# Optimization experiments

Measured on AMD Instinct MI355X. Metric: run time of the kernel, lower is better.

## Reference

```python
import jax, jax.numpy as jnp
import numpy as np

BN_EPS = 1e-5
W_BITS = 2
A_BITS = 2


def _quantize_k(x, k):
    # uniform quantization of x in [0,1] to k bits, straight-through estimator
    n = float(2 ** k - 1)
    q = jnp.round(x * n) / n
    return x + jax.lax.stop_gradient(q - x)


def _quant_weight(w, k):
    # DoReFa-style weight quantization to [-1, 1]
    t = jnp.tanh(w)
    t = t / (2.0 * jnp.max(jnp.abs(t))) + 0.5
    return 2.0 * _quantize_k(t, k) - 1.0


def _quant_act(x, k):
    # DoReFa-style activation quantization: clamp to [0,1], quantize
    return _quantize_k(jnp.clip(x, 0.0, 1.0), k)


def _conv3x3(x, w, stride=1):
    # x: [N,C,H,W], w: [O,I,3,3], padding=1
    return jax.lax.conv_general_dilated(
        x, w, window_strides=(stride, stride), padding=((1, 1), (1, 1)),
        dimension_numbers=('NCHW', 'OIHW', 'NCHW'))


def _bn(x, gamma, beta, mean, var):
    inv = gamma / jnp.sqrt(var + BN_EPS)           # [C]
    return x * inv[None, :, None, None] + (beta - mean * inv)[None, :, None, None]


def setup_inputs() -> dict:
    key = jax.random.key(0)
    ks = jax.random.split(key, 8)
    N, C, H, W = 64, 256, 28, 28
    x = jax.random.normal(ks[0], (N, C, H, W), dtype=jnp.float32)
    w1 = jax.random.normal(ks[1], (C, C, 3, 3), dtype=jnp.float32) * 0.05
    w2 = jax.random.normal(ks[2], (C, C, 3, 3), dtype=jnp.float32) * 0.05
    g1 = jnp.ones((C,), jnp.float32)
    b1 = jnp.zeros((C,), jnp.float32)
    m1 = jax.random.normal(ks[3], (C,), dtype=jnp.float32) * 0.1
    v1 = jax.random.uniform(ks[4], (C,), dtype=jnp.float32) + 0.5
    g2 = jnp.ones((C,), jnp.float32)
    b2 = jnp.zeros((C,), jnp.float32)
    m2 = jax.random.normal(ks[5], (C,), dtype=jnp.float32) * 0.1
    v2 = jax.random.uniform(ks[6], (C,), dtype=jnp.float32) + 0.5
    return {'x': x, 'w1': w1, 'g1': g1, 'b1': b1, 'm1': m1, 'v1': v1,
            'w2': w2, 'g2': g2, 'b2': b2, 'm2': m2, 'v2': v2}


def reference(x, w1, g1, b1, m1, v1, w2, g2, b2, m2, v2):
    residual = x
    # conv1 (2-bit quantized weights & activations) -> bn1 -> relu
    out = _conv3x3(_quant_act(x, A_BITS), _quant_weight(w1, W_BITS), stride=1)
    out = jax.nn.relu(_bn(out, g1, b1, m1, v1))
    # conv2 (2-bit quantized) -> bn2
    out = _conv3x3(_quant_act(out, A_BITS), _quant_weight(w2, W_BITS), stride=1)
    out = _bn(out, g2, b2, m2, v2)
    # residual add + relu
    return jax.nn.relu(out + residual)
```

## Files before the change

kernel.cpp:

```cpp
#include <hip/hip_runtime.h>


#define ABUF 14745600
using i32x4 = __attribute__((ext_vector_type(4))) int;

__device__ __forceinline__ void gload16(const void* g, void* l) {
  typedef const __attribute__((address_space(1))) unsigned int* gp_t;
  typedef __attribute__((address_space(3))) unsigned int* lp_t;
  __builtin_amdgcn_global_load_lds((gp_t)g, (lp_t)l, 16, 0, 0);
}

__global__ void prep_bn(const float* g1, const float* b1, const float* m1, const float* v1,
                        const float* g2, const float* b2, const float* m2, const float* v2,
                        float* s1, float* t1, float* s2, float* t2) {
  int c = threadIdx.x;
  float i1 = g1[c] / sqrtf(v1[c] + 1e-5f);
  s1[c] = i1 * (1.f / 9.f);
  t1[c] = b1[c] - m1[c] * i1;
  float i2 = g2[c] / sqrtf(v2[c] + 1e-5f);
  s2[c] = i2 * (1.f / 9.f);
  t2[c] = b2[c] - m2[c] * i2;
}

__global__ void maxabs_k(const float* __restrict__ w1, const float* __restrict__ w2,
                         unsigned* mx) {
  const float4* v = (const float4*)(blockIdx.y ? w2 : w1);
  float loc = 0.f;
  for (int i = blockIdx.x * 256 + threadIdx.x; i < 147456; i += 65536) {
    float4 f = v[i];
    loc = fmaxf(loc, fmaxf(fmaxf(fabsf(f.x), fabsf(f.y)), fmaxf(fabsf(f.z), fabsf(f.w))));
  }
  #pragma unroll
  for (int off = 32; off; off >>= 1) loc = fmaxf(loc, __shfl_xor(loc, off));
  __shared__ float red[4];
  if ((threadIdx.x & 63) == 0) red[threadIdx.x >> 6] = loc;
  __syncthreads();
  if (threadIdx.x == 0) {
    loc = fmaxf(fmaxf(red[0], red[1]), fmaxf(red[2], red[3]));
    atomicMax(&mx[blockIdx.y], __float_as_uint(loc));
  }
}

__global__ void wquant_k(const float* __restrict__ w1, const float* __restrict__ w2,
                         const unsigned* __restrict__ mx,
                         signed char* __restrict__ wq1, signed char* __restrict__ wq2) {
  const float* w = blockIdx.y ? w2 : w1;
  signed char* o = blockIdx.y ? wq2 : wq1;
  int idx = blockIdx.x * 256 + threadIdx.x;
  int oo = idx / 2304, rr = idx % 2304, t9 = rr >> 8, ci = rr & 255;
  float mt = tanhf(__uint_as_float(mx[blockIdx.y]));
  float t = tanhf(w[oo * 2304 + ci * 9 + t9]) / (2.f * mt) + 0.5f;
  int q = (int)rintf(t * 3.f);
  o[idx] = (signed char)(2 * q - 3);
}

__global__ void aquant_k(const float* __restrict__ x, unsigned char* __restrict__ a1) {
  int n = blockIdx.x / 28, h = blockIdx.x % 28;
  __shared__ __align__(16) unsigned char l[28 * 256];
  int c = threadIdx.x;
  const float4* src = (const float4*)(x + (size_t)(n * 256 + c) * 784 + h * 28);
  #pragma unroll
  for (int i = 0; i < 7; ++i) {
    float4 f = src[i];
    int p = i * 4;
    l[(p + 0) * 256 + c] = (unsigned char)(int)rintf(3.f * fminf(fmaxf(f.x, 0.f), 1.f));
    l[(p + 1) * 256 + c] = (unsigned char)(int)rintf(3.f * fminf(fmaxf(f.y, 0.f), 1.f));
    l[(p + 2) * 256 + c] = (unsigned char)(int)rintf(3.f * fminf(fmaxf(f.z, 0.f), 1.f));
    l[(p + 3) * 256 + c] = (unsigned char)(int)rintf(3.f * fminf(fmaxf(f.w, 0.f), 1.f));
  }
  __syncthreads();
  if (threadIdx.x < 224) {
    int p = threadIdx.x >> 3, q = threadIdx.x & 7;
    const uint4* s = (const uint4*)&l[p * 256 + q * 32];
    uint4 v0 = s[0], v1 = s[1];
    unsigned char* dst = a1 + ((size_t)((n * 30 + h + 1) * 30) + (p + 1)) * 256 + q * 32;
    ((uint4*)dst)[0] = v0;
    ((uint4*)dst)[1] = v1;
  }
}

template <int MODE>
__global__ __launch_bounds__(256, 2) void conv_gemm(
    const unsigned char* __restrict__ act, const signed char* __restrict__ wq,
    const float* __restrict__ sC, const float* __restrict__ tC,
    const float* __restrict__ xres, unsigned char* __restrict__ actout,
    float* __restrict__ fout) {
  __shared__ __align__(16) unsigned char lds[32768];
  const int tid = threadIdx.x;
  const int wv = tid >> 6, lane = tid & 63;
  const int pixBase = blockIdx.x * 128;
  const int wchBase = blockIdx.y * 128;

  int pA[4];
  const signed char* wp[4];
  #pragma unroll
  for (int c = 0; c < 4; ++c) {
    int row = wv * 32 + c * 8 + (lane >> 3);
    int k16 = ((lane & 7) ^ (row & 7)) << 4;
    int m = pixBase + row;
    int n = m / 784, rem = m % 784;
    int hh = rem / 28, ww = rem % 28;
    pA[c] = (((n * 30 + hh) * 30 + ww) << 8) + k16;
    wp[c] = wq + (wchBase + row) * 2304 + k16;
  }

  i32x4 acc[4][4];
  #pragma unroll
  for (int i = 0; i < 4; ++i)
    #pragma unroll
    for (int j = 0; j < 4; ++j) acc[i][j] = (i32x4){0, 0, 0, 0};

  const int prow_off = (MODE == 0) ? (wv & 1) * 64 : (wv >> 1) * 64;
  const int wrow_off = (MODE == 0) ? (wv >> 1) * 64 : (wv & 1) * 64;

  for (int ks = 0; ks < 18; ++ks) {
    const int tap = ks >> 1;
    const int toff = (((tap / 3) * 30 + (tap % 3)) << 8) + ((ks & 1) << 7);
    #pragma unroll
    for (int c = 0; c < 4; ++c) {
      gload16(act + pA[c] + toff, &lds[wv * 4096 + c * 1024]);
      gload16(wp[c] + ks * 128, &lds[16384 + wv * 4096 + c * 1024]);
    }
    __syncthreads();

    i32x4 pf[4][2], wf[4][2];
    #pragma unroll
    for (int f = 0; f < 4; ++f) {
      #pragma unroll
      for (int kc = 0; kc < 2; ++kc) {
        int sl = kc * 4 + (lane >> 4);
        int rp = prow_off + f * 16 + (lane & 15);
        pf[f][kc] = *(const i32x4*)&lds[rp * 128 + ((sl ^ (rp & 7)) << 4)];
        int rw = wrow_off + f * 16 + (lane & 15);
        wf[f][kc] = *(const i32x4*)&lds[16384 + rw * 128 + ((sl ^ (rw & 7)) << 4)];
      }
    }
    #pragma unroll
    for (int kc = 0; kc < 2; ++kc)
      #pragma unroll
      for (int i = 0; i < 4; ++i)
        #pragma unroll
        for (int j = 0; j < 4; ++j) {
          if (MODE == 0)
            acc[i][j] = __builtin_amdgcn_mfma_i32_16x16x64_i8(pf[i][kc], wf[j][kc], acc[i][j], 0, 0, 0);
          else
            acc[i][j] = __builtin_amdgcn_mfma_i32_16x16x64_i8(wf[i][kc], pf[j][kc], acc[i][j], 0, 0, 0);
        }
    __syncthreads();
  }

  if (MODE == 0) {
    #pragma unroll
    for (int j = 0; j < 4; ++j) {
      int c = wchBase + wrow_off + j * 16 + (lane & 15);
      float s = sC[c], t = tC[c];
      #pragma unroll
      for (int i = 0; i < 4; ++i) {
        #pragma unroll
        for (int r = 0; r < 4; ++r) {
          int m = pixBase + prow_off + i * 16 + ((lane >> 4) << 2) + r;
          int n = m / 784, rem = m % 784, hh = rem / 28, ww = rem % 28;
          float y = (float)acc[i][j][r] * s + t;
          y = fminf(fmaxf(y, 0.f), 1.f);
          actout[((n * 30 + hh + 1) * 30 + (ww + 1)) * 256 + c] =
              (unsigned char)(int)rintf(y * 3.f);
        }
      }
    }
  } else {
    #pragma unroll
    for (int i = 0; i < 4; ++i) {
      #pragma unroll
      for (int r = 0; r < 4; ++r) {
        int c = wchBase + wrow_off + i * 16 + ((lane >> 4) << 2) + r;
        float s = sC[c], t = tC[c];
        #pragma unroll
        for (int j = 0; j < 4; ++j) {
          int m = pixBase + prow_off + j * 16 + (lane & 15);
          int n = m / 784, rem = m % 784;
          int addr = n * 200704 + c * 784 + rem;
          float y = (float)acc[i][j][r] * s + t + xres[addr];
          fout[addr] = fmaxf(y, 0.f);
        }
      }
    }
  }
}

extern "C" void kernel_launch(void* const* d_in, const int* in_sizes, int n_in,
                              void* d_out, int out_size, void* d_ws, size_t ws_size,
                              hipStream_t stream) {
  const float* x  = (const float*)d_in[0];
  const float* w1 = (const float*)d_in[1];
  const float* g1 = (const float*)d_in[2];
  const float* b1 = (const float*)d_in[3];
  const float* m1 = (const float*)d_in[4];
  const float* v1 = (const float*)d_in[5];
  const float* w2 = (const float*)d_in[6];
  const float* g2 = (const float*)d_in[7];
  const float* b2 = (const float*)d_in[8];
  const float* m2 = (const float*)d_in[9];
  const float* v2 = (const float*)d_in[10];

  char* ws = (char*)d_ws;
  unsigned* mx = (unsigned*)ws;
  float* s1 = (float*)(ws + 1024);
  float* t1 = (float*)(ws + 2048);
  float* s2 = (float*)(ws + 3072);
  float* t2 = (float*)(ws + 4096);
  unsigned char* a1 = (unsigned char*)(ws + 8192);
  unsigned char* a2 = a1 + ABUF;
  signed char* wq1 = (signed char*)(a2 + ABUF);
  signed char* wq2 = wq1 + 589824;

  hipMemsetAsync(ws, 0, 8192 + 2 * (size_t)ABUF, stream);
  prep_bn<<<1, 256, 0, stream>>>(g1, b1, m1, v1, g2, b2, m2, v2, s1, t1, s2, t2);
  maxabs_k<<<dim3(256, 2), 256, 0, stream>>>(w1, w2, mx);
  wquant_k<<<dim3(2304, 2), 256, 0, stream>>>(w1, w2, mx, wq1, wq2);
  aquant_k<<<64 * 28, 256, 0, stream>>>(x, a1);
  conv_gemm<0><<<dim3(392, 2), 256, 0, stream>>>(a1, wq1, s1, t1, nullptr, a2, nullptr);
  conv_gemm<1><<<dim3(392, 2), 256, 0, stream>>>(a2, wq2, s2, t2, x, nullptr, (float*)d_out);
}
```

Measured before the change: 219.9 us.

## Rewrite conv GEMM as 256x256 double-buffered tile with priority-scheduled phases

Result: slower. 224.7 us (+2.2%).

```diff
diff --git a/kernel.cpp b/kernel.cpp
--- a/kernel.cpp
+++ b/kernel.cpp
@@ -52,6 +52,24 @@
   float t = tanhf(w[oo * 2304 + ci * 9 + t9]) / (2.f * mt) + 0.5f;
   int q = (int)rintf(t * 3.f);
   o[idx] = (signed char)(2 * q - 3);
+}
+
+__global__ void border_zero(unsigned char* __restrict__ a1, unsigned char* __restrict__ a2) {
+  int b = blockIdx.x;
+  unsigned char* base = (b >= 64 ? a2 : a1) + (size_t)(b & 63) * 230400;
+  int tid = threadIdx.x;
+  #pragma unroll
+  for (int it = 0; it < 8; ++it) {
+    int pi = it * 16 + (tid >> 4);
+    if (pi < 116) {
+      int hh, ww;
+      if (pi < 30)      { hh = 0;       ww = pi; }
+      else if (pi < 60) { hh = 29;      ww = pi - 30; }
+      else if (pi < 88) { hh = pi - 59; ww = 0; }
+      else              { hh = pi - 87; ww = 29; }
+      *(uint4*)(base + (hh * 30 + ww) * 256 + (tid & 15) * 16) = uint4{0, 0, 0, 0};
+    }
+  }
 }
 
 __global__ void aquant_k(const float* __restrict__ x, unsigned char* __restrict__ a1) {
@@ -79,104 +97,180 @@
   }
 }
 
+#define PH_MID() do { __builtin_amdgcn_s_barrier(); \
+  asm volatile("s_waitcnt lgkmcnt(0)" ::: "memory"); \
+  __builtin_amdgcn_sched_barrier(0); \
+  __builtin_amdgcn_s_setprio(1); } while (0)
+#define PH_END() do { __builtin_amdgcn_s_setprio(0); \
+  __builtin_amdgcn_s_barrier(); } while (0)
+#define PH_ENDV(N) do { __builtin_amdgcn_s_setprio(0); \
+  asm volatile("s_waitcnt vmcnt(" #N ")" ::: "memory"); \
+  __builtin_amdgcn_sched_barrier(0); \
+  __builtin_amdgcn_s_barrier(); } while (0)
+
 template <int MODE>
-__global__ __launch_bounds__(256, 2) void conv_gemm(
+__global__ __launch_bounds__(512, 2) void conv_gemm(
     const unsigned char* __restrict__ act, const signed char* __restrict__ wq,
     const float* __restrict__ sC, const float* __restrict__ tC,
     const float* __restrict__ xres, unsigned char* __restrict__ actout,
     float* __restrict__ fout) {
-  __shared__ __align__(16) unsigned char lds[32768];
-  const int tid = threadIdx.x;
-  const int wv = tid >> 6, lane = tid & 63;
-  const int pixBase = blockIdx.x * 128;
-  const int wchBase = blockIdx.y * 128;
-
-  int pA[4];
-  const signed char* wp[4];
+  extern __shared__ __align__(16) char lds[];
+  const int tid = threadIdx.x, wv = tid >> 6, lane = tid & 63;
+  const int pixBase = blockIdx.x * 256;
+  const int wvm = wv >> 2, wvn = wv & 3;
+  constexpr int RAoff = (MODE == 0) ? 0 : 32768;
+  constexpr int RBoff = 32768 - RAoff;
+
+  int pixB[2][2], wB[2][2];
+  {
+    int s = (lane & 7) ^ ((lane >> 3) & 7);
+    #pragma unroll
+    for (int h = 0; h < 2; ++h)
+      #pragma unroll
+      for (int c = 0; c < 2; ++c) {
+        int r = h * 128 + c * 64 + wv * 8 + (lane >> 3);
+        int p = pixBase + r;
+        int n = p / 784, rem = p % 784, hh = rem / 28, ww = rem % 28;
+        pixB[h][c] = (((n * 30 + hh) * 30 + ww) << 8) + (s << 4);
+        wB[h][c] = r * 2304 + (s << 4);
+      }
+  }
+  auto tof = [](int kt) {
+    int tap = kt >> 1;
+    return ((tap / 3) * 30 + (tap % 3)) * 256 + ((kt & 1) << 7);
+  };
+  auto stagePix = [&](int h, int kt) {
+    const int base = (kt & 1) * 65536 + h * 16384 + wv * 1024;
+    const int toff = tof(kt);
+    gload16(act + pixB[h][0] + toff, &lds[base]);
+    gload16(act + pixB[h][1] + toff, &lds[base + 8192]);
+  };
+  auto stageW = [&](int h, int kt) {
+    const int base = (kt & 1) * 65536 + 32768 + h * 16384 + wv * 1024;
+    gload16(wq + wB[h][0] + kt * 128, &lds[base]);
+    gload16(wq + wB[h][1] + kt * 128, &lds[base + 8192]);
+  };
+  auto stageA = [&](int h, int kt) { if (MODE == 0) stagePix(h, kt); else stageW(h, kt); };
+  auto stageB = [&](int h, int kt) { if (MODE == 0) stageW(h, kt); else stagePix(h, kt); };
+
+  i32x4 acc[8][4];
   #pragma unroll
-  for (int c = 0; c < 4; ++c) {
-    int row = wv * 32 + c * 8 + (lane >> 3);
-    int k16 = ((lane & 7) ^ (row & 7)) << 4;
-    int m = pixBase + row;
-    int n = m / 784, rem = m % 784;
-    int hh = rem / 28, ww = rem % 28;
-    pA[c] = (((n * 30 + hh) * 30 + ww) << 8) + k16;
-    wp[c] = wq + (wchBase + row) * 2304 + k16;
-  }
-
-  i32x4 acc[4][4];
-  #pragma unroll
-  for (int i = 0; i < 4; ++i)
+  for (int i = 0; i < 8; ++i)
     #pragma unroll
     for (int j = 0; j < 4; ++j) acc[i][j] = (i32x4){0, 0, 0, 0};
-
-  const int prow_off = (MODE == 0) ? (wv & 1) * 64 : (wv >> 1) * 64;
-  const int wrow_off = (MODE == 0) ? (wv >> 1) * 64 : (wv & 1) * 64;
-
-  for (int ks = 0; ks < 18; ++ks) {
-    const int tap = ks >> 1;
-    const int toff = (((tap / 3) * 30 + (tap % 3)) << 8) + ((ks & 1) << 7);
-    #pragma unroll
-    for (int c = 0; c < 4; ++c) {
-      gload16(act + pA[c] + toff, &lds[wv * 4096 + c * 1024]);
-      gload16(wp[c] + ks * 128, &lds[16384 + wv * 4096 + c * 1024]);
-    }
-    __syncthreads();
-
-    i32x4 pf[4][2], wf[4][2];
+  i32x4 pa[4][2], pb0[2][2], pb1[2][2];
+
+  auto rdA = [&](int buf, int mh) {
     #pragma unroll
     for (int f = 0; f < 4; ++f) {
+      int r = wvm * 128 + mh * 64 + f * 16 + (lane & 15);
+      int rb = buf * 65536 + RAoff + r * 128;
       #pragma unroll
       for (int kc = 0; kc < 2; ++kc) {
         int sl = kc * 4 + (lane >> 4);
-        int rp = prow_off + f * 16 + (lane & 15);
-        pf[f][kc] = *(const i32x4*)&lds[rp * 128 + ((sl ^ (rp & 7)) << 4)];
-        int rw = wrow_off + f * 16 + (lane & 15);
-        wf[f][kc] = *(const i32x4*)&lds[16384 + rw * 128 + ((sl ^ (rw & 7)) << 4)];
-      }
-    }
-    #pragma unroll
-    for (int kc = 0; kc < 2; ++kc)
-      #pragma unroll
-      for (int i = 0; i < 4; ++i)
+        pa[f][kc] = *(const i32x4*)&lds[rb + ((sl ^ (r & 7)) << 4)];
+      }
+    }
+  };
+  auto rdB = [&](int buf, int nh, i32x4 (*pb)[2]) {
+    #pragma unroll
+    for (int g = 0; g < 2; ++g) {
+      int r = wvn * 64 + nh * 32 + g * 16 + (lane & 15);
+      int rb = buf * 65536 + RBoff + r * 128;
+      #pragma unroll
+      for (int kc = 0; kc < 2; ++kc) {
+        int sl = kc * 4 + (lane >> 4);
+        pb[g][kc] = *(const i32x4*)&lds[rb + ((sl ^ (r & 7)) << 4)];
+      }
+    }
+  };
+  auto quad = [&](int mh, int nh, i32x4 (*pb)[2]) {
+    #pragma unroll
+    for (int f = 0; f < 4; ++f)
+      #pragma unroll
+      for (int g = 0; g < 2; ++g)
         #pragma unroll
-        for (int j = 0; j < 4; ++j) {
-          if (MODE == 0)
-            acc[i][j] = __builtin_amdgcn_mfma_i32_16x16x64_i8(pf[i][kc], wf[j][kc], acc[i][j], 0, 0, 0);
-          else
-            acc[i][j] = __builtin_amdgcn_mfma_i32_16x16x64_i8(wf[i][kc], pf[j][kc], acc[i][j], 0, 0, 0);
-        }
+        for (int kc = 0; kc < 2; ++kc)
+          acc[mh * 4 + f][nh * 2 + g] = __builtin_amdgcn_mfma_i32_16x16x64_i8(
+              pa[f][kc], pb[g][kc], acc[mh * 4 + f][nh * 2 + g], 0, 0, 0);
+  };
+
+  stageB(0, 0); stageA(0, 0); stageB(1, 0); stageA(1, 0);
+  stageB(0, 1); stageA(0, 1); stageB(1, 1);
+  asm volatile("s_waitcnt vmcnt(6)" ::: "memory");
+  __builtin_amdgcn_sched_barrier(0);
+  __builtin_amdgcn_s_barrier();
+
+  for (int it = 0; it < 9; ++it) {
+    const int ktY = 2 * it + 1, ktX2 = 2 * it + 2, ktY2 = 2 * it + 3;
+    const bool st = (it < 8);
+    rdA(0, 0); rdB(0, 0, pb0);
+    stageA(1, ktY);
+    PH_MID(); quad(0, 0, pb0); PH_END();
+    rdB(0, 1, pb1);
+    PH_MID(); quad(0, 1, pb1); PH_END();
+    rdA(0, 1);
+    if (st) stageB(0, ktX2);
+    PH_MID(); quad(1, 0, pb0); PH_END();
+    if (st) { stageA(0, ktX2); stageB(1, ktX2); }
+    PH_MID(); quad(1, 1, pb1);
+    if (st) { PH_ENDV(6); } else { PH_ENDV(0); }
+    rdA(1, 0); rdB(1, 0, pb0);
+    if (st) stageA(1, ktX2);
+    PH_MID(); quad(0, 0, pb0); PH_END();
+    rdB(1, 1, pb1);
+    PH_MID(); quad(0, 1, pb1); PH_END();
+    rdA(1, 1);
+    if (st) stageB(0, ktY2);
+    PH_MID(); quad(1, 0, pb0); PH_END();
+    if (st) { stageA(0, ktY2); stageB(1, ktY2); }
+    PH_MID(); quad(1, 1, pb1);
+    PH_ENDV(6);
+  }
+
+  if (MODE == 0) {
+    float sj[4], tj[4];
+    #pragma unroll
+    for (int j = 0; j < 4; ++j) {
+      int c = wvn * 64 + j * 16 + (lane & 15);
+      sj[j] = sC[c]; tj[j] = tC[c];
+    }
     __syncthreads();
-  }
-
-  if (MODE == 0) {
-    #pragma unroll
-    for (int j = 0; j < 4; ++j) {
-      int c = wchBase + wrow_off + j * 16 + (lane & 15);
-      float s = sC[c], t = tC[c];
-      #pragma unroll
-      for (int i = 0; i < 4; ++i) {
+    #pragma unroll
+    for (int i = 0; i < 8; ++i) {
+      int lp0 = wvm * 128 + i * 16 + ((lane >> 4) << 2);
+      #pragma unroll
+      for (int j = 0; j < 4; ++j) {
+        int lch = wvn * 64 + j * 16 + (lane & 15);
         #pragma unroll
         for (int r = 0; r < 4; ++r) {
-          int m = pixBase + prow_off + i * 16 + ((lane >> 4) << 2) + r;
-          int n = m / 784, rem = m % 784, hh = rem / 28, ww = rem % 28;
-          float y = (float)acc[i][j][r] * s + t;
+          float y = (float)acc[i][j][r] * sj[j] + tj[j];
           y = fminf(fmaxf(y, 0.f), 1.f);
-          actout[((n * 30 + hh + 1) * 30 + (ww + 1)) * 256 + c] =
-              (unsigned char)(int)rintf(y * 3.f);
+          int lp = lp0 + r;
+          lds[lp * 256 + (lch ^ ((lp & 7) << 4))] = (char)(int)rintf(y * 3.f);
         }
       }
     }
+    __syncthreads();
+    int rr = tid >> 1, hf = tid & 1;
+    int p = pixBase + rr;
+    int n = p / 784, rem = p % 784, hh = rem / 28, ww = rem % 28;
+    unsigned char* dst = actout + (((n * 30 + hh + 1) * 30 + (ww + 1)) << 8) + hf * 128;
+    #pragma unroll
+    for (int k = 0; k < 8; ++k) {
+      uint4 v = *(const uint4*)&lds[rr * 256 + ((hf * 128 + k * 16) ^ ((rr & 7) << 4))];
+      *(uint4*)(dst + k * 16) = v;
+    }
   } else {
     #pragma unroll
-    for (int i = 0; i < 4; ++i) {
+    for (int i = 0; i < 8; ++i) {
       #pragma unroll
       for (int r = 0; r < 4; ++r) {
-        int c = wchBase + wrow_off + i * 16 + ((lane >> 4) << 2) + r;
+        int c = wvm * 128 + i * 16 + ((lane >> 4) << 2) + r;
         float s = sC[c], t = tC[c];
         #pragma unroll
         for (int j = 0; j < 4; ++j) {
-          int m = pixBase + prow_off + j * 16 + (lane & 15);
+          int m = pixBase + wvn * 64 + j * 16 + (lane & 15);
           int n = m / 784, rem = m % 784;
           int addr = n * 200704 + c * 784 + rem;
           float y = (float)acc[i][j][r] * s + t + xres[addr];
@@ -213,11 +307,19 @@
   signed char* wq1 = (signed char*)(a2 + ABUF);
   signed char* wq2 = wq1 + 589824;
 
-  hipMemsetAsync(ws, 0, 8192 + 2 * (size_t)ABUF, stream);
+  void (*k0)(const unsigned char*, const signed char*, const float*, const float*,
+             const float*, unsigned char*, float*) = conv_gemm<0>;
+  void (*k1)(const unsigned char*, const signed char*, const float*, const float*,
+             const float*, unsigned char*, float*) = conv_gemm<1>;
+  hipFuncSetAttribute((const void*)k0, hipFuncAttributeMaxDynamicSharedMemorySize, 131072);
+  hipFuncSetAttribute((const void*)k1, hipFuncAttributeMaxDynamicSharedMemorySize, 131072);
+
+  hipMemsetAsync(ws, 0, 1024, stream);
   prep_bn<<<1, 256, 0, stream>>>(g1, b1, m1, v1, g2, b2, m2, v2, s1, t1, s2, t2);
   maxabs_k<<<dim3(256, 2), 256, 0, stream>>>(w1, w2, mx);
   wquant_k<<<dim3(2304, 2), 256, 0, stream>>>(w1, w2, mx, wq1, wq2);
+  border_zero<<<128, 256, 0, stream>>>(a1, a2);
   aquant_k<<<64 * 28, 256, 0, stream>>>(x, a1);
-  conv_gemm<0><<<dim3(392, 2), 256, 0, stream>>>(a1, wq1, s1, t1, nullptr, a2, nullptr);
-  conv_gemm<1><<<dim3(392, 2), 256, 0, stream>>>(a2, wq2, s2, t2, x, nullptr, (float*)d_out);
-}
+  conv_gemm<0><<<196, 512, 131072, stream>>>(a1, wq1, s1, t1, nullptr, a2, nullptr);
+  conv_gemm<1><<<196, 512, 131072, stream>>>(a2, wq2, s2, t2, x, nullptr, (float*)d_out);
+}
```
